# Optimization experiments

Hardware: AMD Instinct MI355X
Metric: run time of the kernel (lower is better)

## Reference

```python
import jax, jax.numpy as jnp
import numpy as np

B, N, C, H = 32, 577, 768, 12
D = C // H  # head dim 64
HID = 3072  # hardcoded Mlp hidden
ALPHA = 0.1
EPS = 1e-6


def setup_inputs() -> dict:
    key = jax.random.key(0)
    ks = jax.random.split(key, 8)
    s = 0.02
    return {
        "x": jax.random.normal(ks[0], (B, N, C), jnp.float32),
        "attn_weight": jax.random.uniform(ks[1], (B, N - 1), jnp.float32),
        "ln1_w": jnp.ones((C,), jnp.float32),
        "ln1_b": jnp.zeros((C,), jnp.float32),
        "qkv_w": jax.random.normal(ks[2], (3 * C, C), jnp.float32) * s,
        "qkv_b": jnp.zeros((3 * C,), jnp.float32),
        "proj_w": jax.random.normal(ks[3], (C, C), jnp.float32) * s,
        "proj_b": jnp.zeros((C,), jnp.float32),
        "ln2_w": jnp.ones((C,), jnp.float32),
        "ln2_b": jnp.zeros((C,), jnp.float32),
        "fc1_w": jax.random.normal(ks[4], (HID, C), jnp.float32) * s,
        "fc1_b": jnp.zeros((HID,), jnp.float32),
        "fc2_w": jax.random.normal(ks[5], (C, HID), jnp.float32) * s,
        "fc2_b": jnp.zeros((C,), jnp.float32),
    }


def _ln(x, w, b):
    m = x.mean(-1, keepdims=True)
    v = jnp.var(x, axis=-1, keepdims=True)
    return (x - m) * jax.lax.rsqrt(v + EPS) * w + b


def reference(x, attn_weight, ln1_w, ln1_b, qkv_w, qkv_b, proj_w, proj_b,
              ln2_w, ln2_b, fc1_w, fc1_b, fc2_w, fc2_b):
    h = _ln(x, ln1_w, ln1_b)
    qkv = (h @ qkv_w.T + qkv_b).reshape(B, N, 3, H, D)
    q = qkv[:, :, 0].transpose(0, 2, 1, 3)  # [B,H,N,D]
    k = qkv[:, :, 1].transpose(0, 2, 1, 3)
    v = qkv[:, :, 2].transpose(0, 2, 1, 3)
    scale = D ** -0.5
    attn = jnp.einsum('bhnd,bhmd->bhnm', q, k) * scale  # [B,H,N,N]
    patch_attn = attn[:, :, 0, 1:]  # pre-reweight CLS->patch scores
    # multiplicative reweighting of CLS row (cols 1:) before softmax
    factor = jnp.concatenate(
        [jnp.ones((B, 1), attn.dtype), attn_weight * ALPHA + (1.0 - ALPHA)], axis=-1)
    attn = attn.at[:, :, 0, :].multiply(factor[:, None, :])
    attn = jax.nn.softmax(attn, axis=-1)
    out = jnp.einsum('bhnm,bhmd->bhnd', attn, v)
    out = out.transpose(0, 2, 1, 3).reshape(B, N, C)
    out = out @ proj_w.T + proj_b
    x = x + out
    h2 = _ln(x, ln2_w, ln2_b)
    h2 = jax.nn.gelu(h2 @ fc1_w.T + fc1_b, approximate=False)  # nn.GELU exact
    h2 = h2 @ fc2_w.T + fc2_b
    x = x + h2
    return (x, patch_attn)
```

## Files before the change

kernel.cpp:

```cpp
#include <hip/hip_runtime.h>
#include <hip/hip_bf16.h>
#include <cstdint>

#define BB 32
#define NN 577
#define CC 768
#define HH 12
#define HIDN 3072
#define MROWS (BB*NN)

typedef __attribute__((ext_vector_type(8))) short bf16x8;
typedef __attribute__((ext_vector_type(4))) float f32x4;

__device__ __forceinline__ float b2f(unsigned short u) {
    union { float f; unsigned int i; } x; x.i = ((unsigned int)u) << 16; return x.f;
}
__device__ __forceinline__ unsigned short f2b(float f) {
    union { float f; unsigned int i; } x; x.f = f;
    unsigned int i = x.i;
    i += 0x7fffu + ((i >> 16) & 1u);
    return (unsigned short)(i >> 16);
}

__device__ __forceinline__ void async16(const void* g, void* l) {
    __builtin_amdgcn_global_load_lds(
        (const __attribute__((address_space(1))) uint32_t*)g,
        (__attribute__((address_space(3))) uint32_t*)l, 16, 0, 0);
}

__device__ __forceinline__ float gelu_f(float v) {
    float ax = fabsf(v) * 0.70710678118654752f;
    float t = __builtin_amdgcn_rcpf(1.0f + 0.3275911f * ax);
    float poly = t * (0.254829592f + t * (-0.284496736f + t * (1.421413741f +
                 t * (-1.453152027f + t * 1.061405429f))));
    float e = __expf(-ax * ax);
    float erf_abs = 1.0f - poly * e;
    float erf_v = (v >= 0.f) ? erf_abs : -erf_abs;
    return 0.5f * v * (1.0f + erf_v);
}

__global__ void cvt4(const float* __restrict__ a, int na, unsigned short* __restrict__ oa,
                     const float* __restrict__ b, int nb, unsigned short* __restrict__ ob,
                     const float* __restrict__ c, int nc, unsigned short* __restrict__ oc,
                     const float* __restrict__ d, int nd, unsigned short* __restrict__ od) {
    int stride = gridDim.x * blockDim.x;
    int t = blockIdx.x * blockDim.x + threadIdx.x;
    for (int i = t; i < (na >> 2); i += stride) {
        float4 f = ((const float4*)a)[i];
        ushort4 o = { f2b(f.x), f2b(f.y), f2b(f.z), f2b(f.w) };
        ((ushort4*)oa)[i] = o;
    }
    for (int i = t; i < (nb >> 2); i += stride) {
        float4 f = ((const float4*)b)[i];
        ushort4 o = { f2b(f.x), f2b(f.y), f2b(f.z), f2b(f.w) };
        ((ushort4*)ob)[i] = o;
    }
    for (int i = t; i < (nc >> 2); i += stride) {
        float4 f = ((const float4*)c)[i];
        ushort4 o = { f2b(f.x), f2b(f.y), f2b(f.z), f2b(f.w) };
        ((ushort4*)oc)[i] = o;
    }
    for (int i = t; i < (nd >> 2); i += stride) {
        float4 f = ((const float4*)d)[i];
        ushort4 o = { f2b(f.x), f2b(f.y), f2b(f.z), f2b(f.w) };
        ((ushort4*)od)[i] = o;
    }
}

__global__ __launch_bounds__(256)
void ln_kernel(const float* __restrict__ x, const float* __restrict__ w,
               const float* __restrict__ bsv, unsigned short* __restrict__ out) {
    const int lane = threadIdx.x & 63, wv = threadIdx.x >> 6;
    const int row = blockIdx.x * 4 + wv;
    const float* xr = x + (size_t)row * CC;
    float4 v[3]; float s = 0.f, ss = 0.f;
    #pragma unroll
    for (int i = 0; i < 3; ++i) {
        v[i] = *(const float4*)&xr[(lane + i * 64) * 4];
        s  += v[i].x + v[i].y + v[i].z + v[i].w;
        ss += v[i].x * v[i].x + v[i].y * v[i].y + v[i].z * v[i].z + v[i].w * v[i].w;
    }
    #pragma unroll
    for (int off = 32; off; off >>= 1) { s += __shfl_xor(s, off); ss += __shfl_xor(ss, off); }
    float m = s * (1.0f / 768.0f);
    float r = rsqrtf(ss * (1.0f / 768.0f) - m * m + 1e-6f);
    #pragma unroll
    for (int i = 0; i < 3; ++i) {
        int c = (lane + i * 64) * 4;
        float4 wv4 = *(const float4*)&w[c];
        float4 bv4 = *(const float4*)&bsv[c];
        ushort4 o;
        o.x = f2b((v[i].x - m) * r * wv4.x + bv4.x);
        o.y = f2b((v[i].y - m) * r * wv4.y + bv4.y);
        o.z = f2b((v[i].z - m) * r * wv4.z + bv4.z);
        o.w = f2b((v[i].w - m) * r * wv4.w + bv4.w);
        *(ushort4*)&out[(size_t)row * CC + c] = o;
    }
}

template <int EPI>
__global__ __launch_bounds__(256, 4)
void gemm_bt(const unsigned short* __restrict__ A, const unsigned short* __restrict__ Bw,
             const float* __restrict__ bias, const float* __restrict__ resid,
             unsigned short* __restrict__ outb, float* __restrict__ outf,
             int M, int N, int K) {
    const int NT = gridDim.x;
    const int MT = (M + 127) >> 7;
    int flat = blockIdx.y * NT + blockIdx.x;
    int xcd = flat & 7, s = flat >> 3;
    int n_t = s % NT, mj = s / NT;
    int m_t = xcd + 8 * mj;
    if (m_t >= MT) return;
    const int m0 = m_t * 128, n0 = n_t * 128;

    __shared__ __align__(16) unsigned short As[2][128 * 32];
    __shared__ __align__(16) unsigned short Bs[2][128 * 32];
    const int tid = threadIdx.x;
    const int wave = tid >> 6, lane = tid & 63;
    const int wr = wave >> 1, wc = wave & 1;
    const int quad = lane >> 4, l16 = lane & 15;

    f32x4 acc[4][4] = {};

    const int c0 = tid, c1 = 256 + tid;
    const int row0 = c0 >> 2, seg0 = c0 & 3;
    const int row1 = c1 >> 2, seg1 = c1 & 3;
    int gm0 = m0 + row0; if (gm0 > M - 1) gm0 = M - 1;
    int gm1 = m0 + row1; if (gm1 > M - 1) gm1 = M - 1;
    const unsigned short* a0 = A + (size_t)gm0 * K + seg0 * 8;
    const unsigned short* a1 = A + (size_t)gm1 * K + seg1 * 8;
    const unsigned short* b0 = Bw + (size_t)(n0 + row0) * K + seg0 * 8;
    const unsigned short* b1 = Bw + (size_t)(n0 + row1) * K + seg1 * 8;

    for (int k0 = 0; k0 < K; k0 += 64) {
        #pragma unroll
        for (int p = 0; p < 2; ++p) {
            int kk = k0 + p * 32;
            async16(a0 + kk, &As[p][c0 * 8]);
            async16(a1 + kk, &As[p][c1 * 8]);
            async16(b0 + kk, &Bs[p][c0 * 8]);
            async16(b1 + kk, &Bs[p][c1 * 8]);
        }
        __syncthreads();
        #pragma unroll
        for (int p = 0; p < 2; ++p) {
            bf16x8 bfr[4];
            #pragma unroll
            for (int ni = 0; ni < 4; ++ni)
                bfr[ni] = *(const bf16x8*)&Bs[p][(wc * 64 + ni * 16 + l16) * 32 + quad * 8];
            #pragma unroll
            for (int mi = 0; mi < 4; ++mi) {
                bf16x8 af = *(const bf16x8*)&As[p][(wr * 64 + mi * 16 + l16) * 32 + quad * 8];
                #pragma unroll
                for (int ni = 0; ni < 4; ++ni)
                    acc[mi][ni] = __builtin_amdgcn_mfma_f32_16x16x32_bf16(af, bfr[ni], acc[mi][ni], 0, 0, 0);
            }
        }
        __syncthreads();
    }

    #pragma unroll
    for (int mi = 0; mi < 4; ++mi) {
        #pragma unroll
        for (int r = 0; r < 4; ++r) {
            int grow = m0 + wr * 64 + mi * 16 + quad * 4 + r;
            if (grow >= M) continue;
            #pragma unroll
            for (int ni = 0; ni < 4; ++ni) {
                int gcol = n0 + wc * 64 + ni * 16 + l16;
                float v = acc[mi][ni][r] + bias[gcol];
                size_t idx = (size_t)grow * N + gcol;
                if (EPI == 0) {
                    outb[idx] = f2b(v);
                } else if (EPI == 1) {
                    outb[idx] = f2b(gelu_f(v));
                } else {
                    outf[idx] = resid[idx] + v;
                }
            }
        }
    }
}

__global__ __launch_bounds__(256)
void attn_mfma(const unsigned short* __restrict__ qkv, const float* __restrict__ aw,
               unsigned short* __restrict__ O, float* __restrict__ patch) {
    const int qt = blockIdx.x, h = blockIdx.y, b = blockIdx.z;
    const int tid = threadIdx.x, wv = tid >> 6, lane = tid & 63;
    const int quad = lane >> 4, l16 = lane & 15;

    __shared__ __align__(16) unsigned short Ks[64 * 72];
    __shared__ __align__(16) unsigned short Vt[64 * 72];
    __shared__ __align__(16) unsigned short Pt[4][16 * 72];

    int qrow = qt * 64 + wv * 16 + l16;
    int qclamp = qrow < NN ? qrow : NN - 1;
    const unsigned short* qbase = qkv + (size_t)(b * NN + qclamp) * 2304 + h * 64;
    bf16x8 qf[2];
    qf[0] = *(const bf16x8*)(qbase + quad * 8);
    qf[1] = *(const bf16x8*)(qbase + 32 + quad * 8);
    #pragma unroll
    for (int i = 0; i < 2; ++i) {
        union { bf16x8 v; unsigned short u[8]; } t; t.v = qf[i];
        #pragma unroll
        for (int j = 0; j < 8; ++j) t.u[j] = f2b(b2f(t.u[j]) * 0.125f);
        qf[i] = t.v;
    }

    union { bf16x8 v; unsigned short u[8]; } onesf;
    #pragma unroll
    for (int j = 0; j < 8; ++j) onesf.u[j] = (l16 == 0) ? (unsigned short)0x3F80 : (unsigned short)0;

    f32x4 o[4] = {};
    f32x4 o5 = {};
    float mst[4];
    #pragma unroll
    for (int r = 0; r < 4; ++r) mst[r] = -1.0e30f;

    int keyc[2], segc[2], swzc[2];
    const unsigned short* kb_base;
    const unsigned short* vb_base;
    {
        int c0 = tid, c1 = 256 + tid;
        keyc[0] = c0 >> 3; segc[0] = c0 & 7;
        keyc[1] = c1 >> 3; segc[1] = c1 & 7;
        #pragma unroll
        for (int i = 0; i < 2; ++i) {
            int kg = keyc[i] >> 3, kl = keyc[i] & 7;
            swzc[i] = (kg ^ segc[i]) * 8 + kl;
        }
        kb_base = qkv + (size_t)b * NN * 2304 + 768 + h * 64;
        vb_base = qkv + (size_t)b * NN * 2304 + 1536 + h * 64;
    }

    bf16x8 pk[2], pv[2];
    #pragma unroll
    for (int i = 0; i < 2; ++i) {
        int gk = keyc[i]; if (gk >= NN) gk = NN - 1;
        pk[i] = *(const bf16x8*)(kb_base + (size_t)gk * 2304 + segc[i] * 8);
        pv[i] = *(const bf16x8*)(vb_base + (size_t)gk * 2304 + segc[i] * 8);
    }

    for (int kt = 0; kt < 10; ++kt) {
        __syncthreads();
        #pragma unroll
        for (int i = 0; i < 2; ++i) {
            *(bf16x8*)&Ks[keyc[i] * 72 + segc[i] * 8] = pk[i];
            union { bf16x8 v; unsigned short u[8]; } t; t.v = pv[i];
            #pragma unroll
            for (int e = 0; e < 8; ++e)
                Vt[(segc[i] * 8 + e) * 72 + swzc[i]] = t.u[e];
        }
        __syncthreads();

        if (kt < 9) {
            #pragma unroll
            for (int i = 0; i < 2; ++i) {
                int gk = (kt + 1) * 64 + keyc[i]; if (gk >= NN) gk = NN - 1;
                pk[i] = *(const bf16x8*)(kb_base + (size_t)gk * 2304 + segc[i] * 8);
                pv[i] = *(const bf16x8*)(vb_base + (size_t)gk * 2304 + segc[i] * 8);
            }
        }

        f32x4 s[4];
        __builtin_amdgcn_s_setprio(1);
        #pragma unroll
        for (int ni = 0; ni < 4; ++ni) {
            bf16x8 b0 = *(const bf16x8*)&Ks[(ni * 16 + l16) * 72 + quad * 8];
            bf16x8 b1 = *(const bf16x8*)&Ks[(ni * 16 + l16) * 72 + 32 + quad * 8];
            f32x4 acc = {};
            acc = __builtin_amdgcn_mfma_f32_16x16x32_bf16(qf[0], b0, acc, 0, 0, 0);
            acc = __builtin_amdgcn_mfma_f32_16x16x32_bf16(qf[1], b1, acc, 0, 0, 0);
            s[ni] = acc;
        }
        __builtin_amdgcn_s_setprio(0);

        if (kt == 9) {
            #pragma unroll
            for (int ni = 0; ni < 4; ++ni) {
                if (ni * 16 + l16 != 0) {
                    #pragma unroll
                    for (int r = 0; r < 4; ++r) s[ni][r] = -1.0e30f;
                }
            }
        }

        if (qt == 0 && wv == 0 && quad == 0) {
            #pragma unroll
            for (int ni = 0; ni < 4; ++ni) {
                int gkey = kt * 64 + ni * 16 + l16;
                if (gkey >= 1 && gkey < NN) {
                    patch[(size_t)(b * HH + h) * (NN - 1) + gkey - 1] = s[ni][0];
                    float f = aw[b * (NN - 1) + gkey - 1] * 0.1f + 0.9f;
                    s[ni][0] *= f;
                }
            }
        }

        float al[4];
        #pragma unroll
        for (int r = 0; r < 4; ++r) {
            float tm = fmaxf(fmaxf(s[0][r], s[1][r]), fmaxf(s[2][r], s[3][r]));
            tm = fmaxf(tm, __shfl_xor(tm, 1));
            tm = fmaxf(tm, __shfl_xor(tm, 2));
            tm = fmaxf(tm, __shfl_xor(tm, 4));
            tm = fmaxf(tm, __shfl_xor(tm, 8));
            float nm = fmaxf(mst[r], tm);
            al[r] = __expf(mst[r] - nm);
            mst[r] = nm;
        }
        #pragma unroll
        for (int r = 0; r < 4; ++r) {
            #pragma unroll
            for (int ni = 0; ni < 4; ++ni) {
                float p = __expf(s[ni][r] - mst[r]);
                Pt[wv][(quad * 4 + r) * 72 + ni * 16 + l16] = f2b(p);
            }
            #pragma unroll
            for (int ni = 0; ni < 4; ++ni) o[ni][r] *= al[r];
            o5[r] *= al[r];
        }

        __builtin_amdgcn_s_setprio(1);
        #pragma unroll
        for (int kc = 0; kc < 2; ++kc) {
            bf16x8 af = *(const bf16x8*)&Pt[wv][l16 * 72 + kc * 32 + quad * 8];
            #pragma unroll
            for (int ni = 0; ni < 4; ++ni) {
                int d = ni * 16 + l16;
                int gs = (kc * 4 + quad) ^ (d >> 3);
                bf16x8 vf = *(const bf16x8*)&Vt[d * 72 + gs * 8];
                o[ni] = __builtin_amdgcn_mfma_f32_16x16x32_bf16(af, vf, o[ni], 0, 0, 0);
            }
            o5 = __builtin_amdgcn_mfma_f32_16x16x32_bf16(af, onesf.v, o5, 0, 0, 0);
        }
        __builtin_amdgcn_s_setprio(0);
    }

    #pragma unroll
    for (int r = 0; r < 4; ++r) {
        float lr = __shfl(o5[r], quad << 4);
        float inv = (lr > 0.f) ? __builtin_amdgcn_rcpf(lr) : 0.f;
        int row = qt * 64 + wv * 16 + quad * 4 + r;
        if (row < NN) {
            #pragma unroll
            for (int ni = 0; ni < 4; ++ni)
                O[(size_t)(b * NN + row) * CC + h * 64 + ni * 16 + l16] = f2b(o[ni][r] * inv);
        }
    }
}

extern "C" void kernel_launch(void* const* d_in, const int* in_sizes, int n_in,
                              void* d_out, int out_size, void* d_ws, size_t ws_size,
                              hipStream_t stream) {
    const float* x       = (const float*)d_in[0];
    const float* aw      = (const float*)d_in[1];
    const float* ln1w    = (const float*)d_in[2];
    const float* ln1b    = (const float*)d_in[3];
    const float* qkvw_f  = (const float*)d_in[4];
    const float* qkvb    = (const float*)d_in[5];
    const float* projw_f = (const float*)d_in[6];
    const float* projb   = (const float*)d_in[7];
    const float* ln2w    = (const float*)d_in[8];
    const float* ln2b    = (const float*)d_in[9];
    const float* fc1w_f  = (const float*)d_in[10];
    const float* fc1b    = (const float*)d_in[11];
    const float* fc2w_f  = (const float*)d_in[12];
    const float* fc2b    = (const float*)d_in[13];

    char* ws = (char*)d_ws;
    unsigned short* h_bf  = (unsigned short*)(ws + 0);
    unsigned short* qkv   = (unsigned short*)(ws + 28360704);
    unsigned short* g1    = (unsigned short*)(ws + 0);
    unsigned short* attno = (unsigned short*)(ws + 113442816);
    float*          x1    = (float*)(ws + 141803520);
    unsigned short* h2    = (unsigned short*)(ws + 198524928);
    unsigned short* qkvw  = (unsigned short*)(ws + 226885632);
    unsigned short* projw = (unsigned short*)(ws + 230424576);
    unsigned short* fc1w  = (unsigned short*)(ws + 231604224);
    unsigned short* fc2w  = (unsigned short*)(ws + 236322816);

    float* out_x = (float*)d_out;
    float* out_patch = out_x + (size_t)MROWS * CC;

    cvt4<<<1024, 256, 0, stream>>>(qkvw_f, 2304 * 768, qkvw,
                                   projw_f, 768 * 768, projw,
                                   fc1w_f, 3072 * 768, fc1w,
                                   fc2w_f, 768 * 3072, fc2w);
    ln_kernel<<<MROWS / 4, 256, 0, stream>>>(x, ln1w, ln1b, h_bf);
    gemm_bt<0><<<dim3(18, 152), 256, 0, stream>>>(h_bf, qkvw, qkvb, nullptr, qkv, nullptr,
                                                  MROWS, 2304, 768);
    attn_mfma<<<dim3(10, HH, BB), 256, 0, stream>>>(qkv, aw, attno, out_patch);
    gemm_bt<2><<<dim3(6, 152), 256, 0, stream>>>(attno, projw, projb, x, nullptr, x1,
                                                 MROWS, 768, 768);
    ln_kernel<<<MROWS / 4, 256, 0, stream>>>(x1, ln2w, ln2b, h2);
    gemm_bt<1><<<dim3(24, 152), 256, 0, stream>>>(h2, fc1w, fc1b, nullptr, g1, nullptr,
                                                  MROWS, 3072, 768);
    gemm_bt<2><<<dim3(6, 152), 256, 0, stream>>>(g1, fc2w, fc2b, x1, nullptr, out_x,
                                                 MROWS, 768, 3072);
}
```

Before: 669.9 us.

## Process two 64-row query groups per attention block to reuse K/V tiles

Each attention block now handles 128 query rows as two independent online-softmax states that share every staged K/V tile in LDS, and the grid is halved along the query dimension. This halves global K/V reads and LDS staging work per query row. In exchange it roughly doubles accumulator registers per thread, which may reduce occupancy, and leaves fewer blocks for load balancing.

```diff
diff --git a/kernel.cpp b/kernel.cpp
--- a/kernel.cpp
+++ b/kernel.cpp
@@ -182,40 +182,145 @@
     }
 }
 
+struct AttnState {
+    bf16x8 qf[2];
+    f32x4 o[4];
+    f32x4 o5;
+    float mst[4];
+};
+
+__device__ __forceinline__ void attn_load_q(AttnState& st, const unsigned short* qkv,
+                                            int b, int h, int row, int quad) {
+    int qclamp = row < NN ? row : NN - 1;
+    const unsigned short* qbase = qkv + (size_t)(b * NN + qclamp) * 2304 + h * 64;
+    st.qf[0] = *(const bf16x8*)(qbase + quad * 8);
+    st.qf[1] = *(const bf16x8*)(qbase + 32 + quad * 8);
+    #pragma unroll
+    for (int i = 0; i < 2; ++i) {
+        union { bf16x8 v; unsigned short u[8]; } t; t.v = st.qf[i];
+        #pragma unroll
+        for (int j = 0; j < 8; ++j) t.u[j] = f2b(b2f(t.u[j]) * 0.125f);
+        st.qf[i] = t.v;
+    }
+    #pragma unroll
+    for (int r = 0; r < 4; ++r) { st.o[r] = f32x4{}; st.mst[r] = -1.0e30f; }
+    st.o5 = f32x4{};
+}
+
+__device__ __forceinline__ void attn_group(AttnState& st,
+    const unsigned short* Ks, const unsigned short* Vt, unsigned short* PtW,
+    int quad, int l16, bf16x8 ones, bool lastTile,
+    bool doPatch, int kt, int b, int h, const float* __restrict__ aw,
+    float* __restrict__ patch) {
+    f32x4 s[4];
+    __builtin_amdgcn_s_setprio(1);
+    #pragma unroll
+    for (int ni = 0; ni < 4; ++ni) {
+        bf16x8 b0 = *(const bf16x8*)&Ks[(ni * 16 + l16) * 72 + quad * 8];
+        bf16x8 b1 = *(const bf16x8*)&Ks[(ni * 16 + l16) * 72 + 32 + quad * 8];
+        f32x4 acc = {};
+        acc = __builtin_amdgcn_mfma_f32_16x16x32_bf16(st.qf[0], b0, acc, 0, 0, 0);
+        acc = __builtin_amdgcn_mfma_f32_16x16x32_bf16(st.qf[1], b1, acc, 0, 0, 0);
+        s[ni] = acc;
+    }
+    __builtin_amdgcn_s_setprio(0);
+
+    if (lastTile) {
+        #pragma unroll
+        for (int ni = 0; ni < 4; ++ni) {
+            if (ni * 16 + l16 != 0) {
+                #pragma unroll
+                for (int r = 0; r < 4; ++r) s[ni][r] = -1.0e30f;
+            }
+        }
+    }
+
+    if (doPatch) {
+        #pragma unroll
+        for (int ni = 0; ni < 4; ++ni) {
+            int gkey = kt * 64 + ni * 16 + l16;
+            if (gkey >= 1 && gkey < NN) {
+                patch[(size_t)(b * HH + h) * (NN - 1) + gkey - 1] = s[ni][0];
+                float f = aw[b * (NN - 1) + gkey - 1] * 0.1f + 0.9f;
+                s[ni][0] *= f;
+            }
+        }
+    }
+
+    float al[4];
+    #pragma unroll
+    for (int r = 0; r < 4; ++r) {
+        float tm = fmaxf(fmaxf(s[0][r], s[1][r]), fmaxf(s[2][r], s[3][r]));
+        tm = fmaxf(tm, __shfl_xor(tm, 1));
+        tm = fmaxf(tm, __shfl_xor(tm, 2));
+        tm = fmaxf(tm, __shfl_xor(tm, 4));
+        tm = fmaxf(tm, __shfl_xor(tm, 8));
+        float nm = fmaxf(st.mst[r], tm);
+        al[r] = __expf(st.mst[r] - nm);
+        st.mst[r] = nm;
+    }
+    #pragma unroll
+    for (int r = 0; r < 4; ++r) {
+        #pragma unroll
+        for (int ni = 0; ni < 4; ++ni) {
+            float p = __expf(s[ni][r] - st.mst[r]);
+            PtW[(quad * 4 + r) * 72 + ni * 16 + l16] = f2b(p);
+        }
+        #pragma unroll
+        for (int ni = 0; ni < 4; ++ni) st.o[ni][r] *= al[r];
+        st.o5[r] *= al[r];
+    }
+
+    __builtin_amdgcn_s_setprio(1);
+    #pragma unroll
+    for (int kc = 0; kc < 2; ++kc) {
+        bf16x8 af = *(const bf16x8*)&PtW[l16 * 72 + kc * 32 + quad * 8];
+        #pragma unroll
+        for (int ni = 0; ni < 4; ++ni) {
+            int d = ni * 16 + l16;
+            int gs = (kc * 4 + quad) ^ (d >> 3);
+            bf16x8 vf = *(const bf16x8*)&Vt[d * 72 + gs * 8];
+            st.o[ni] = __builtin_amdgcn_mfma_f32_16x16x32_bf16(af, vf, st.o[ni], 0, 0, 0);
+        }
+        st.o5 = __builtin_amdgcn_mfma_f32_16x16x32_bf16(af, ones, st.o5, 0, 0, 0);
+    }
+    __builtin_amdgcn_s_setprio(0);
+}
+
+__device__ __forceinline__ void attn_store(const AttnState& st, unsigned short* __restrict__ O,
+                                           int b, int h, int rowBase, int quad, int l16) {
+    #pragma unroll
+    for (int r = 0; r < 4; ++r) {
+        float lr = __shfl(st.o5[r], quad << 4);
+        float inv = (lr > 0.f) ? __builtin_amdgcn_rcpf(lr) : 0.f;
+        int row = rowBase + quad * 4 + r;
+        if (row < NN) {
+            #pragma unroll
+            for (int ni = 0; ni < 4; ++ni)
+                O[(size_t)(b * NN + row) * CC + h * 64 + ni * 16 + l16] = f2b(st.o[ni][r] * inv);
+        }
+    }
+}
+
 __global__ __launch_bounds__(256)
 void attn_mfma(const unsigned short* __restrict__ qkv, const float* __restrict__ aw,
                unsigned short* __restrict__ O, float* __restrict__ patch) {
     const int qt = blockIdx.x, h = blockIdx.y, b = blockIdx.z;
     const int tid = threadIdx.x, wv = tid >> 6, lane = tid & 63;
     const int quad = lane >> 4, l16 = lane & 15;
+    const int qb = qt * 128;
 
     __shared__ __align__(16) unsigned short Ks[64 * 72];
     __shared__ __align__(16) unsigned short Vt[64 * 72];
     __shared__ __align__(16) unsigned short Pt[4][16 * 72];
 
-    int qrow = qt * 64 + wv * 16 + l16;
-    int qclamp = qrow < NN ? qrow : NN - 1;
-    const unsigned short* qbase = qkv + (size_t)(b * NN + qclamp) * 2304 + h * 64;
-    bf16x8 qf[2];
-    qf[0] = *(const bf16x8*)(qbase + quad * 8);
-    qf[1] = *(const bf16x8*)(qbase + 32 + quad * 8);
-    #pragma unroll
-    for (int i = 0; i < 2; ++i) {
-        union { bf16x8 v; unsigned short u[8]; } t; t.v = qf[i];
-        #pragma unroll
-        for (int j = 0; j < 8; ++j) t.u[j] = f2b(b2f(t.u[j]) * 0.125f);
-        qf[i] = t.v;
-    }
+    AttnState stA, stB;
+    attn_load_q(stA, qkv, b, h, qb + wv * 16 + l16, quad);
+    attn_load_q(stB, qkv, b, h, qb + 64 + wv * 16 + l16, quad);
 
     union { bf16x8 v; unsigned short u[8]; } onesf;
     #pragma unroll
     for (int j = 0; j < 8; ++j) onesf.u[j] = (l16 == 0) ? (unsigned short)0x3F80 : (unsigned short)0;
-
-    f32x4 o[4] = {};
-    f32x4 o5 = {};
-    float mst[4];
-    #pragma unroll
-    for (int r = 0; r < 4; ++r) mst[r] = -1.0e30f;
 
     int keyc[2], segc[2], swzc[2];
     const unsigned short* kb_base;
@@ -241,6 +346,8 @@
         pv[i] = *(const bf16x8*)(vb_base + (size_t)gk * 2304 + segc[i] * 8);
     }
 
+    const bool patchLane = (qt == 0 && wv == 0 && quad == 0);
+
     for (int kt = 0; kt < 10; ++kt) {
         __syncthreads();
         #pragma unroll
@@ -262,92 +369,15 @@
             }
         }
 
-        f32x4 s[4];
-        __builtin_amdgcn_s_setprio(1);
-        #pragma unroll
-        for (int ni = 0; ni < 4; ++ni) {
-            bf16x8 b0 = *(const bf16x8*)&Ks[(ni * 16 + l16) * 72 + quad * 8];
-            bf16x8 b1 = *(const bf16x8*)&Ks[(ni * 16 + l16) * 72 + 32 + quad * 8];
-            f32x4 acc = {};
-            acc = __builtin_amdgcn_mfma_f32_16x16x32_bf16(qf[0], b0, acc, 0, 0, 0);
-            acc = __builtin_amdgcn_mfma_f32_16x16x32_bf16(qf[1], b1, acc, 0, 0, 0);
-            s[ni] = acc;
-        }
-        __builtin_amdgcn_s_setprio(0);
-
-        if (kt == 9) {
-            #pragma unroll
-            for (int ni = 0; ni < 4; ++ni) {
-                if (ni * 16 + l16 != 0) {
-                    #pragma unroll
-                    for (int r = 0; r < 4; ++r) s[ni][r] = -1.0e30f;
-                }
-            }
-        }
-
-        if (qt == 0 && wv == 0 && quad == 0) {
-            #pragma unroll
-            for (int ni = 0; ni < 4; ++ni) {
-                int gkey = kt * 64 + ni * 16 + l16;
-                if (gkey >= 1 && gkey < NN) {
-                    patch[(size_t)(b * HH + h) * (NN - 1) + gkey - 1] = s[ni][0];
-                    float f = aw[b * (NN - 1) + gkey - 1] * 0.1f + 0.9f;
-                    s[ni][0] *= f;
-                }
-            }
-        }
-
-        float al[4];
-        #pragma unroll
-        for (int r = 0; r < 4; ++r) {
-            float tm = fmaxf(fmaxf(s[0][r], s[1][r]), fmaxf(s[2][r], s[3][r]));
-            tm = fmaxf(tm, __shfl_xor(tm, 1));
-            tm = fmaxf(tm, __shfl_xor(tm, 2));
-            tm = fmaxf(tm, __shfl_xor(tm, 4));
-            tm = fmaxf(tm, __shfl_xor(tm, 8));
-            float nm = fmaxf(mst[r], tm);
-            al[r] = __expf(mst[r] - nm);
-            mst[r] = nm;
-        }
-        #pragma unroll
-        for (int r = 0; r < 4; ++r) {
-            #pragma unroll
-            for (int ni = 0; ni < 4; ++ni) {
-                float p = __expf(s[ni][r] - mst[r]);
-                Pt[wv][(quad * 4 + r) * 72 + ni * 16 + l16] = f2b(p);
-            }
-            #pragma unroll
-            for (int ni = 0; ni < 4; ++ni) o[ni][r] *= al[r];
-            o5[r] *= al[r];
-        }
-
-        __builtin_amdgcn_s_setprio(1);
-        #pragma unroll
-        for (int kc = 0; kc < 2; ++kc) {
-            bf16x8 af = *(const bf16x8*)&Pt[wv][l16 * 72 + kc * 32 + quad * 8];
-            #pragma unroll
-            for (int ni = 0; ni < 4; ++ni) {
-                int d = ni * 16 + l16;
-                int gs = (kc * 4 + quad) ^ (d >> 3);
-                bf16x8 vf = *(const bf16x8*)&Vt[d * 72 + gs * 8];
-                o[ni] = __builtin_amdgcn_mfma_f32_16x16x32_bf16(af, vf, o[ni], 0, 0, 0);
-            }
-            o5 = __builtin_amdgcn_mfma_f32_16x16x32_bf16(af, onesf.v, o5, 0, 0, 0);
-        }
-        __builtin_amdgcn_s_setprio(0);
-    }
-
-    #pragma unroll
-    for (int r = 0; r < 4; ++r) {
-        float lr = __shfl(o5[r], quad << 4);
-        float inv = (lr > 0.f) ? __builtin_amdgcn_rcpf(lr) : 0.f;
-        int row = qt * 64 + wv * 16 + quad * 4 + r;
-        if (row < NN) {
-            #pragma unroll
-            for (int ni = 0; ni < 4; ++ni)
-                O[(size_t)(b * NN + row) * CC + h * 64 + ni * 16 + l16] = f2b(o[ni][r] * inv);
-        }
-    }
+        const bool last = (kt == 9);
+        attn_group(stA, Ks, Vt, Pt[wv], quad, l16, onesf.v, last,
+                   patchLane, kt, b, h, aw, patch);
+        attn_group(stB, Ks, Vt, Pt[wv], quad, l16, onesf.v, last,
+                   false, kt, b, h, aw, patch);
+    }
+
+    attn_store(stA, O, b, h, qb + wv * 16, quad, l16);
+    attn_store(stB, O, b, h, qb + 64 + wv * 16, quad, l16);
 }
 
 extern "C" void kernel_launch(void* const* d_in, const int* in_sizes, int n_in,
@@ -390,7 +420,7 @@
     ln_kernel<<<MROWS / 4, 256, 0, stream>>>(x, ln1w, ln1b, h_bf);
     gemm_bt<0><<<dim3(18, 152), 256, 0, stream>>>(h_bf, qkvw, qkvb, nullptr, qkv, nullptr,
                                                   MROWS, 2304, 768);
-    attn_mfma<<<dim3(10, HH, BB), 256, 0, stream>>>(qkv, aw, attno, out_patch);
+    attn_mfma<<<dim3(5, HH, BB), 256, 0, stream>>>(qkv, aw, attno, out_patch);
     gemm_bt<2><<<dim3(6, 152), 256, 0, stream>>>(attno, projw, projb, x, nullptr, x1,
                                                  MROWS, 768, 768);
     ln_kernel<<<MROWS / 4, 256, 0, stream>>>(x1, ln2w, ln2b, h2);
```

Result: slower. 706.4 us (+5.4%).

## Add 256x256-tile MFMA GEMM with XCD-aware block mapping for MLP layers

Applied to the files above, without the earlier changes.

Adds a new bf16 MFMA GEMM kernel with 256x256 output tiles, 512 threads and a 128KB double-buffered LDS pipeline. It overlaps async global-to-LDS loads with compute, raises wave priority during the MFMA loop, and remaps block indices so M-tiles are grouped per XCD. The fc1 and fc2 GEMMs now use it instead of the 128-tile kernel. The goal is more reuse per loaded tile and better L2 locality, at the cost of higher register and LDS pressure and lower occupancy.

```diff
diff --git a/kernel.cpp b/kernel.cpp
--- a/kernel.cpp
+++ b/kernel.cpp
@@ -169,6 +169,116 @@
             for (int ni = 0; ni < 4; ++ni) {
                 int gcol = n0 + wc * 64 + ni * 16 + l16;
                 float v = acc[mi][ni][r] + bias[gcol];
+                size_t idx = (size_t)grow * N + gcol;
+                if (EPI == 0) {
+                    outb[idx] = f2b(v);
+                } else if (EPI == 1) {
+                    outb[idx] = f2b(gelu_f(v));
+                } else {
+                    outf[idx] = resid[idx] + v;
+                }
+            }
+        }
+    }
+}
+
+template <int EPI>
+__global__ __launch_bounds__(512, 2)
+void gemm_bt256(const unsigned short* __restrict__ A, const unsigned short* __restrict__ Bw,
+                const float* __restrict__ bias, const float* __restrict__ resid,
+                unsigned short* __restrict__ outb, float* __restrict__ outf,
+                int M, int N, int K) {
+    const int NT = gridDim.x;
+    const int MT = (M + 255) >> 8;
+    int flat = blockIdx.y * NT + blockIdx.x;
+    int xcd = flat & 7, s = flat >> 3;
+    int n_t = s % NT, mj = s / NT;
+    int m_t = xcd + 8 * mj;
+    if (m_t >= MT) return;
+    const int m0 = m_t * 256, n0 = n_t * 256;
+
+    extern __shared__ __align__(16) unsigned short smem[];
+    unsigned short* As = smem;
+    unsigned short* Bs = smem + 32768;
+
+    const int tid = threadIdx.x;
+    const int wave = tid >> 6, lane = tid & 63;
+    const int quad = lane >> 4, l16 = lane & 15;
+    const int wm = wave >> 2, wn = wave & 3;
+
+    f32x4 acc[8][4] = {};
+
+    const int R = tid >> 2, sg = tid & 3;
+    int amr0 = m0 + R;       if (amr0 > M - 1) amr0 = M - 1;
+    int amr1 = m0 + R + 128; if (amr1 > M - 1) amr1 = M - 1;
+    const unsigned short* aP0 = A + (size_t)amr0 * K + sg * 8;
+    const unsigned short* aP1 = A + (size_t)amr1 * K + sg * 8;
+    const unsigned short* bP0 = Bw + (size_t)(n0 + R) * K + sg * 8;
+    const unsigned short* bP1 = Bw + (size_t)(n0 + R + 128) * K + sg * 8;
+
+    const int T = K >> 6;
+
+    #pragma unroll
+    for (int h = 0; h < 2; ++h) {
+        int ko = h * 32;
+        unsigned short* la = As + h * 8192;
+        unsigned short* lb = Bs + h * 8192;
+        async16(aP0 + ko, la + tid * 8);
+        async16(aP1 + ko, la + (512 + tid) * 8);
+        async16(bP0 + ko, lb + tid * 8);
+        async16(bP1 + ko, lb + (512 + tid) * 8);
+    }
+    asm volatile("s_waitcnt vmcnt(4)" ::: "memory");
+    __builtin_amdgcn_s_barrier();
+
+    for (int t = 0; t < T; ++t) {
+        const int cur = t & 1, nb = cur ^ 1;
+        const bool lastt = (t + 1 == T);
+        #pragma unroll
+        for (int h = 0; h < 2; ++h) {
+            bf16x8 afr[8], bfr[4];
+            const unsigned short* la = As + ((cur << 1) + h) * 8192;
+            const unsigned short* lb = Bs + ((cur << 1) + h) * 8192;
+            #pragma unroll
+            for (int mi = 0; mi < 8; ++mi)
+                afr[mi] = *(const bf16x8*)&la[(wm * 128 + mi * 16 + l16) * 32 + quad * 8];
+            #pragma unroll
+            for (int nj = 0; nj < 4; ++nj)
+                bfr[nj] = *(const bf16x8*)&lb[(wn * 64 + nj * 16 + l16) * 32 + quad * 8];
+            if (!lastt) {
+                int ko = (t + 1) * 64 + h * 32;
+                unsigned short* sa = As + ((nb << 1) + h) * 8192;
+                unsigned short* sb = Bs + ((nb << 1) + h) * 8192;
+                async16(aP0 + ko, sa + tid * 8);
+                async16(aP1 + ko, sa + (512 + tid) * 8);
+                async16(bP0 + ko, sb + tid * 8);
+                async16(bP1 + ko, sb + (512 + tid) * 8);
+                asm volatile("s_waitcnt vmcnt(4)" ::: "memory");
+            } else if (h == 0) {
+                asm volatile("s_waitcnt vmcnt(0)" ::: "memory");
+            }
+            __builtin_amdgcn_s_barrier();
+            __builtin_amdgcn_s_setprio(1);
+            #pragma unroll
+            for (int mi = 0; mi < 8; ++mi)
+                #pragma unroll
+                for (int nj = 0; nj < 4; ++nj)
+                    acc[mi][nj] = __builtin_amdgcn_mfma_f32_16x16x32_bf16(afr[mi], bfr[nj], acc[mi][nj], 0, 0, 0);
+            __builtin_amdgcn_s_setprio(0);
+            __builtin_amdgcn_s_barrier();
+        }
+    }
+
+    #pragma unroll
+    for (int mi = 0; mi < 8; ++mi) {
+        #pragma unroll
+        for (int r = 0; r < 4; ++r) {
+            int grow = m0 + wm * 128 + mi * 16 + quad * 4 + r;
+            if (grow >= M) continue;
+            #pragma unroll
+            for (int nj = 0; nj < 4; ++nj) {
+                int gcol = n0 + wn * 64 + nj * 16 + l16;
+                float v = acc[mi][nj][r] + bias[gcol];
                 size_t idx = (size_t)grow * N + gcol;
                 if (EPI == 0) {
                     outb[idx] = f2b(v);
@@ -394,8 +504,8 @@
     gemm_bt<2><<<dim3(6, 152), 256, 0, stream>>>(attno, projw, projb, x, nullptr, x1,
                                                  MROWS, 768, 768);
     ln_kernel<<<MROWS / 4, 256, 0, stream>>>(x1, ln2w, ln2b, h2);
-    gemm_bt<1><<<dim3(24, 152), 256, 0, stream>>>(h2, fc1w, fc1b, nullptr, g1, nullptr,
-                                                  MROWS, 3072, 768);
-    gemm_bt<2><<<dim3(6, 152), 256, 0, stream>>>(g1, fc2w, fc2b, x1, nullptr, out_x,
-                                                 MROWS, 768, 3072);
-}
+    gemm_bt256<1><<<dim3(12, 80), 512, 131072, stream>>>(h2, fc1w, fc1b, nullptr, g1, nullptr,
+                                                         MROWS, 3072, 768);
+    gemm_bt256<2><<<dim3(3, 80), 512, 131072, stream>>>(g1, fc2w, fc2b, x1, nullptr, out_x,
+                                                        MROWS, 768, 3072);
+}
```

After: 675.9 us. About the same (+0.9%).
